# Performance work log

Hardware: AMD Instinct MI355X
Metric: run time of the kernel (lower is better)

## Reference

```python
import math
import jax, jax.numpy as jnp
import numpy as np

B, I, D, H, K, MAXI, FF = 2, 1024, 1024, 16, 64, 1024, 4096
DH = D // H
EPS = 1e-5

def _ln(x, g, b):
    m = x.mean(-1, keepdims=True)
    v = ((x - m) ** 2).mean(-1, keepdims=True)
    return (x - m) / jnp.sqrt(v + EPS) * g + b

def setup_inputs() -> dict:
    key = jax.random.key(0)
    ks = jax.random.split(key, 16)
    p = lambda i, sh: (0.02 * jax.random.normal(ks[i], sh)).astype(jnp.float32)
    # clamped relative-position indices: clamp(j - floor(1.0*i), -K, K) + K
    ar = np.arange(MAXI)
    idx = np.clip(ar[None, :] - ar[:, None], -K, K) + K  # [maxI, maxI]
    return {
        'x': jax.random.normal(ks[0], (B, I, D), dtype=jnp.float32),
        'j': jax.random.normal(ks[1], (B, I, D), dtype=jnp.float32),
        'ln1_g': jnp.ones((D,), jnp.float32), 'ln1_b': jnp.zeros((D,), jnp.float32),
        'Wv_w': p(2, (D, D)), 'Wv_b': jnp.zeros((D,), jnp.float32),
        'Wg_w': p(3, (D, D)), 'Wg_b': jnp.zeros((D,), jnp.float32),
        'lnv_g': jnp.ones((D,), jnp.float32), 'lnv_b': jnp.zeros((D,), jnp.float32),
        'Wq1_w': p(4, (D, D)), 'Wq1_b': jnp.zeros((D,), jnp.float32),
        'Wk_w': p(5, (D, D)), 'Wk_b': jnp.zeros((D,), jnp.float32),
        'Wq2_w': p(6, (D, D)), 'Wq2_b': jnp.zeros((D,), jnp.float32),
        'rel_emb': p(7, (2 * K + 1, D)),
        'Wo_w': p(8, (D, D)), 'Wo_b': jnp.zeros((D,), jnp.float32),
        'ln2_g': jnp.ones((D,), jnp.float32), 'ln2_b': jnp.zeros((D,), jnp.float32),
        'ff1_w': p(9, (D, FF)), 'ff1_b': jnp.zeros((FF,), jnp.float32),
        'ff2_w': p(10, (FF, D)), 'ff2_b': jnp.zeros((D,), jnp.float32),
        'indices': jnp.asarray(idx, jnp.int32),
    }

def reference(x, j, ln1_g, ln1_b, Wv_w, Wv_b, Wg_w, Wg_b, lnv_g, lnv_b,
              Wq1_w, Wq1_b, Wk_w, Wk_b, Wq2_w, Wq2_b, rel_emb,
              Wo_w, Wo_b, ln2_g, ln2_b, ff1_w, ff1_b, ff2_w, ff2_b, indices):
    Bv, Iq, _ = x.shape
    res = x
    xn = _ln(x, ln1_g, ln1_b)
    # value / gate streams with gelu activation, layernorm on v only
    v = _ln(jax.nn.gelu(xn @ Wv_w + Wv_b, approximate=False), lnv_g, lnv_b)
    g = jax.nn.gelu(xn @ Wg_w + Wg_b, approximate=False)
    vh = v.reshape(Bv, -1, H, DH)   # [B,J,H,Dh]
    gh = g.reshape(Bv, -1, H, DH)   # [B,I,H,Dh]
    # absolute-position scores: Q1(j) . K(j)^T
    q1 = (j @ Wq1_w + Wq1_b).reshape(Bv, -1, H, DH)
    kh = (j @ Wk_w + Wk_b).reshape(Bv, -1, H, DH)
    aa = jnp.einsum('bihd,bjhd->bhij', q1, kh)  # [B,H,I,J]
    # relative-position scores: Q2(j) . rel_embed^T, gathered by clamped indices
    q2 = (j @ Wq2_w + Wq2_b).reshape(Bv, -1, H, DH)
    rh = rel_emb.reshape(2 * K + 1, H, DH)
    arf = jnp.einsum('bihd,rhd->bhir', q2, rh)  # [B,H,I,2K+1]
    Jk = kh.shape[1]
    idx = jnp.broadcast_to(indices[None, None, :Iq, :Jk], (Bv, H, Iq, Jk))
    ar = jnp.take_along_axis(arf, idx, axis=-1)  # [B,H,I,J]
    a = jax.nn.softmax((aa + ar) / math.sqrt(DH), axis=-1)
    o = jnp.einsum('bhij,bjhd->bihd', a, vh) * gh  # gated attention output
    o = o.reshape(Bv, -1, D) @ Wo_w + Wo_b
    x1 = o + res
    # feed-forward sublayer
    h = jax.nn.relu(_ln(x1, ln2_g, ln2_b) @ ff1_w + ff1_b)
    out = h @ ff2_w + ff2_b + x1
    return (out, a)
```

## Files before the change

kernel.cpp:

```cpp
#include <hip/hip_runtime.h>
#include <hip/hip_bf16.h>
#include <math.h>

#define D_   1024
#define H_   16
#define DH_  64
#define FF_  4096
#define R_   129
#define I_   1024
#define B_   2
#define MROWS 2048
#define QKVLD 3072

typedef __bf16 v8bf16 __attribute__((ext_vector_type(8)));
typedef float f32x4 __attribute__((ext_vector_type(4)));

__device__ __forceinline__ float gelu_f(float x) {
    return 0.5f * x * (1.0f + erff(x * 0.7071067811865476f));
}

__device__ __forceinline__ void ldsld16(const void* g, void* l) {
    __builtin_amdgcn_global_load_lds(
        (const __attribute__((address_space(1))) void*)g,
        (__attribute__((address_space(3))) void*)l, 16, 0, 0);
}

__global__ __launch_bounds__(256) void cvt_bf16(const float* __restrict__ in,
        __hip_bfloat16* __restrict__ out, int n4) {
    int i = blockIdx.x * 256 + threadIdx.x;
    if (i >= n4) return;
    float4 v = reinterpret_cast<const float4*>(in)[i];
    union { __hip_bfloat16 h[4]; uint2 u; } pk;
    pk.h[0] = __float2bfloat16(v.x); pk.h[1] = __float2bfloat16(v.y);
    pk.h[2] = __float2bfloat16(v.z); pk.h[3] = __float2bfloat16(v.w);
    reinterpret_cast<uint2*>(out)[i] = pk.u;
}

__global__ __launch_bounds__(256) void cvt_rel_bias(const float* __restrict__ rel,
        __hip_bfloat16* __restrict__ relb,
        const float* __restrict__ q1b_, const float* __restrict__ kb_,
        const float* __restrict__ q2b_, const float* __restrict__ vb_,
        const float* __restrict__ gb_,
        float* __restrict__ bias3, float* __restrict__ bias2) {
    int bid = blockIdx.x, t = threadIdx.x;
    if (bid < 129) {
        int i = bid * 256 + t;
        float4 v = reinterpret_cast<const float4*>(rel)[i];
        union { __hip_bfloat16 h[4]; uint2 u; } pk;
        pk.h[0] = __float2bfloat16(v.x); pk.h[1] = __float2bfloat16(v.y);
        pk.h[2] = __float2bfloat16(v.z); pk.h[3] = __float2bfloat16(v.w);
        reinterpret_cast<uint2*>(relb)[i] = pk.u;
    } else {
        int k = bid - 129;
        const float* src = k == 0 ? q1b_ : k == 1 ? kb_ : k == 2 ? q2b_ : k == 3 ? vb_ : gb_;
        float* dst = (k < 3 ? bias3 + k * D_ : bias2 + (k - 3) * D_);
        reinterpret_cast<float4*>(dst)[t] = reinterpret_cast<const float4*>(src)[t];
    }
}

__global__ __launch_bounds__(256) void wtrans6(
        const float* __restrict__ s0, const float* __restrict__ s1,
        const float* __restrict__ s2, const float* __restrict__ s3,
        const float* __restrict__ s4, const float* __restrict__ s5,
        __hip_bfloat16* __restrict__ d0, __hip_bfloat16* __restrict__ d1,
        __hip_bfloat16* __restrict__ d2, __hip_bfloat16* __restrict__ d3,
        __hip_bfloat16* __restrict__ d4, __hip_bfloat16* __restrict__ d5) {
    __shared__ float T[64][65];
    int z = blockIdx.z;
    const float* W = z == 0 ? s0 : z == 1 ? s1 : z == 2 ? s2 : z == 3 ? s3 : z == 4 ? s4 : s5;
    __hip_bfloat16* WT = z == 0 ? d0 : z == 1 ? d1 : z == 2 ? d2 : z == 3 ? d3 : z == 4 ? d4 : d5;
    int k0 = blockIdx.y * 64, n0 = blockIdx.x * 64;
    int t = threadIdx.x;
#pragma unroll
    for (int i = 0; i < 16; i++) {
        int e = t + i * 256, r = e >> 6, c = e & 63;
        T[r][c] = W[(size_t)(k0 + r) * D_ + n0 + c];
    }
    __syncthreads();
#pragma unroll
    for (int i = 0; i < 16; i++) {
        int e = t + i * 256, r = e >> 6, c = e & 63;
        WT[(size_t)(n0 + r) * D_ + k0 + c] = __float2bfloat16(T[c][r]);
    }
}

__global__ __launch_bounds__(256) void wtrans_ff(
        const float* __restrict__ f1, const float* __restrict__ f2,
        __hip_bfloat16* __restrict__ d1, __hip_bfloat16* __restrict__ d2) {
    __shared__ float T[64][65];
    int z = blockIdx.z;
    const float* W = z == 0 ? f1 : f2;
    __hip_bfloat16* WT = z == 0 ? d1 : d2;
    int K = z == 0 ? D_ : FF_;
    int N = z == 0 ? FF_ : D_;
    int k0 = (z == 0 ? blockIdx.y : blockIdx.x) * 64;
    int n0 = (z == 0 ? blockIdx.x : blockIdx.y) * 64;
    int t = threadIdx.x;
#pragma unroll
    for (int i = 0; i < 16; i++) {
        int e = t + i * 256, r = e >> 6, c = e & 63;
        T[r][c] = W[(size_t)(k0 + r) * N + n0 + c];
    }
    __syncthreads();
#pragma unroll
    for (int i = 0; i < 16; i++) {
        int e = t + i * 256, r = e >> 6, c = e & 63;
        WT[(size_t)(n0 + r) * K + k0 + c] = __float2bfloat16(T[c][r]);
    }
}

__global__ __launch_bounds__(256) void vtrans(const float* __restrict__ v,
        __hip_bfloat16* __restrict__ vt) {
    __shared__ float T[64][65];
    int z = blockIdx.y, b = z >> 4, h = z & 15;
    int j0 = blockIdx.x * 64;
    int t = threadIdx.x;
#pragma unroll
    for (int i = 0; i < 16; i++) {
        int e = t + i * 256, r = e >> 6, c = e & 63;
        T[r][c] = v[(size_t)(b * I_ + j0 + r) * D_ + h * DH_ + c];
    }
    __syncthreads();
#pragma unroll
    for (int i = 0; i < 16; i++) {
        int e = t + i * 256, r = e >> 6, c = e & 63;
        vt[((size_t)z * DH_ + r) * I_ + j0 + c] = __float2bfloat16(T[c][r]);
    }
}

template<int MR, int NWC, int ACT, int RES, int OUTBF>
__global__ __launch_bounds__(256) void gemm_mfma(
        const __hip_bfloat16* __restrict__ A,
        const __hip_bfloat16* __restrict__ Bt,
        const float* __restrict__ bias,
        const float* __restrict__ res,
        void* __restrict__ Cout,
        int N, int Kd, int lda, int ldb, int ldc,
        size_t sAb, size_t sAh, size_t sBb, size_t sBh, size_t sCz) {
    constexpr int NWR = 4 / NWC;
    constexpr int BM = NWR * MR * 16;
    constexpr int BN = NWC * 64;
    __shared__ __align__(16) __hip_bfloat16 As[BM * 64];
    __shared__ __align__(16) __hip_bfloat16 Bs[BN * 64];
    const char* AsB = (const char*)As;
    const char* BsB = (const char*)Bs;
    int z = blockIdx.z;
    const __hip_bfloat16* Ab = A + (size_t)(z >> 4) * sAb + (size_t)(z & 15) * sAh;
    const __hip_bfloat16* Bb = Bt + (size_t)(z >> 4) * sBb + (size_t)(z & 15) * sBh;
    float* Cf = (float*)Cout + (size_t)z * sCz;
    __hip_bfloat16* Cb = (__hip_bfloat16*)Cout + (size_t)z * sCz;
    int m0 = blockIdx.y * BM, n0 = blockIdx.x * BN;
    int t = threadIdx.x;
    int l = t & 63, w = t >> 6;
    int wr = w / NWC, wc = w % NWC;
    int lr = l & 15, kq = l >> 4;
    int rx = lr & 7;

    f32x4 acc[MR][4] = {};

    for (int k0 = 0; k0 < Kd; k0 += 64) {
#pragma unroll
        for (int i = 0; i < BM / 32; i++) {
            int e = t + i * 256;
            int row = e >> 3, sl = e & 7;
            int kb = sl ^ (row & 7);
            ldsld16(Ab + (size_t)(m0 + row) * lda + (k0 + kb * 8), (void*)(AsB + e * 16));
        }
#pragma unroll
        for (int i = 0; i < BN / 32; i++) {
            int e = t + i * 256;
            int row = e >> 3, sl = e & 7;
            int kb = sl ^ (row & 7);
            int nr = n0 + row; if (nr > N - 1) nr = N - 1;
            ldsld16(Bb + (size_t)nr * ldb + (k0 + kb * 8), (void*)(BsB + e * 16));
        }
        __syncthreads();
#pragma unroll
        for (int kc = 0; kc < 2; kc++) {
            int sloff = (((kc << 2) + kq) ^ rx) << 4;
            v8bf16 af[MR], bfr[4];
#pragma unroll
            for (int mr = 0; mr < MR; mr++)
                af[mr] = *(const v8bf16*)(AsB + ((wr * (MR * 16) + mr * 16 + lr) << 7) + sloff);
#pragma unroll
            for (int nc = 0; nc < 4; nc++)
                bfr[nc] = *(const v8bf16*)(BsB + ((wc * 64 + nc * 16 + lr) << 7) + sloff);
#pragma unroll
            for (int mr = 0; mr < MR; mr++)
#pragma unroll
                for (int nc = 0; nc < 4; nc++)
                    acc[mr][nc] = __builtin_amdgcn_mfma_f32_16x16x32_bf16(
                        af[mr], bfr[nc], acc[mr][nc], 0, 0, 0);
        }
        __syncthreads();
    }

#pragma unroll
    for (int mr = 0; mr < MR; mr++) {
        int rbase = m0 + wr * (MR * 16) + mr * 16 + kq * 4;
#pragma unroll
        for (int nc = 0; nc < 4; nc++) {
            int col = n0 + wc * 64 + nc * 16 + lr;
            bool okc = col < N;
            float bv = (bias && okc) ? bias[col] : 0.f;
#pragma unroll
            for (int ri = 0; ri < 4; ri++) {
                int r = rbase + ri;
                float val = acc[mr][nc][ri] + bv;
                if (ACT == 1) val = gelu_f(val);
                if (ACT == 2) val = fmaxf(val, 0.f);
                if (RES) val += res[(size_t)r * ldc + col];
                if (okc) {
                    if (OUTBF == 2) {
                        if (col < D_) Cf[(size_t)r * ldc + col] = val;
                        else ((__hip_bfloat16*)res)[(size_t)r * ldc + (col - D_)] =
                                 __float2bfloat16(val);
                    } else if (OUTBF == 1) {
                        Cb[(size_t)r * ldc + col] = __float2bfloat16(val);
                    } else {
                        Cf[(size_t)r * ldc + col] = val;
                    }
                }
            }
        }
    }
}

#define F5_K  32512
#define F5_V  40704
#define F5_P  48896
#define SC2   0.1803368801111244f
__global__ __launch_bounds__(512) void flash_attn5(
        const __hip_bfloat16* __restrict__ qkv,
        const __hip_bfloat16* __restrict__ vt,
        const __hip_bfloat16* __restrict__ arfb,
        const __hip_bfloat16* __restrict__ gb,
        float* __restrict__ a_out,
        __hip_bfloat16* __restrict__ obuf) {
    __shared__ __align__(16) char lds[65280];
    __hip_bfloat16* arl = (__hip_bfloat16*)lds;
    char* kB = lds + F5_K;
    char* vB = lds + F5_V;
    char* pB = lds + F5_P;

    int z = blockIdx.y, b = z >> 4, h = z & 15;
    int i0 = blockIdx.x * 128;
    int t = threadIdx.x, l = t & 63, w = t >> 6;
    int lr = l & 15, kq = l >> 4;
    const __hip_bfloat16* Kg = qkv + (size_t)(b * I_) * QKVLD + D_ + h * DH_;
    const __hip_bfloat16* Vg = vt + (size_t)z * DH_ * I_;
    const __hip_bfloat16* arz = arfb + (size_t)z * I_ * R_;

#pragma unroll
    for (int i = 0; i < 2; i++) {
        int e = t + i * 512;
        int row = e >> 3, sl = e & 7;
        int kb = sl ^ (row & 7);
        ldsld16(qkv + (size_t)(b * I_ + i0 + row) * QKVLD + h * DH_ + kb * 8,
                (void*)(pB + e * 16));
    }
    for (int idx = t; idx < 128 * 127; idx += 512) {
        int row = idx / 127, rm = idx - row * 127;
        arl[idx] = arz[((size_t)(i0 + row)) * R_ + rm + 1];
    }
    __syncthreads();
    v8bf16 qf[2];
#pragma unroll
    for (int kc = 0; kc < 2; kc++)
        qf[kc] = *(const v8bf16*)(pB + ((w * 16 + lr) << 7) + ((((kc << 2) + kq) ^ (lr & 7)) << 4));

    int irow = w * 16 + kq * 4;
    int ig = i0 + irow;
    float loS[4], hiS[4];
#pragma unroll
    for (int ri = 0; ri < 4; ri++) {
        loS[ri] = __bfloat162float(arz[((size_t)(ig + ri)) * R_ + 0])   * SC2;
        hiS[ri] = __bfloat162float(arz[((size_t)(ig + ri)) * R_ + 128]) * SC2;
    }

    float l_ln[4] = {0.f, 0.f, 0.f, 0.f};
    for (int jt = 0; jt < 16; jt++) {
        int j0 = jt * 64;
        {
            int row = t >> 3, sl = t & 7;
            int kb = sl ^ (row & 7);
            ldsld16(Kg + (size_t)(j0 + row) * QKVLD + kb * 8, (void*)(kB + t * 16));
        }
        __syncthreads();
        f32x4 acc[4] = {};
        __builtin_amdgcn_s_setprio(1);
#pragma unroll
        for (int kc = 0; kc < 2; kc++) {
            int sloff = ((((kc << 2) + kq)) ^ (lr & 7)) << 4;
#pragma unroll
            for (int tt = 0; tt < 4; tt++) {
                v8bf16 kf = *(const v8bf16*)(kB + ((tt * 16 + lr) << 7) + sloff);
                acc[tt] = __builtin_amdgcn_mfma_f32_16x16x32_bf16(qf[kc], kf, acc[tt], 0, 0, 0);
            }
        }
        __builtin_amdgcn_s_setprio(0);
#pragma unroll
        for (int ri = 0; ri < 4; ri++) {
            int i_g = ig + ri;
            float sc[4];
            bool lo_all = (j0 + 63) <= (i_g - 64);
            bool hi_all = j0 >= (i_g + 64);
            if (lo_all || hi_all) {
                float c = lo_all ? loS[ri] : hiS[ri];
#pragma unroll
                for (int tt = 0; tt < 4; tt++) sc[tt] = fmaf(acc[tt][ri], SC2, c);
            } else {
#pragma unroll
                for (int tt = 0; tt < 4; tt++) {
                    int reln = j0 + tt * 16 + lr - i_g;
                    float arv = reln <= -64 ? loS[ri] : (reln >= 64 ? hiS[ri] :
                        __bfloat162float(arl[(irow + ri) * 127 + reln + 63]) * SC2);
                    sc[tt] = fmaf(acc[tt][ri], SC2, arv);
                }
            }
            l_ln[ri] += exp2f(sc[0]) + exp2f(sc[1]) + exp2f(sc[2]) + exp2f(sc[3]);
        }
        __syncthreads();
    }
    float offb[4];
#pragma unroll
    for (int ri = 0; ri < 4; ri++) {
        float s = l_ln[ri];
#pragma unroll
        for (int off = 1; off < 16; off <<= 1) s += __shfl_xor(s, off, 64);
        offb[ri] = __log2f(s);
    }

    f32x4 oacc[4] = {};
    for (int jt = 0; jt < 16; jt++) {
        int j0 = jt * 64;
        {
            int row = t >> 3, sl = t & 7;
            int kb = sl ^ (row & 7);
            ldsld16(Kg + (size_t)(j0 + row) * QKVLD + kb * 8, (void*)(kB + t * 16));
            ldsld16(Vg + (size_t)row * I_ + j0 + kb * 8, (void*)(vB + t * 16));
        }
        __syncthreads();
        f32x4 acc[4] = {};
        __builtin_amdgcn_s_setprio(1);
#pragma unroll
        for (int kc = 0; kc < 2; kc++) {
            int sloff = ((((kc << 2) + kq)) ^ (lr & 7)) << 4;
#pragma unroll
            for (int tt = 0; tt < 4; tt++) {
                v8bf16 kf = *(const v8bf16*)(kB + ((tt * 16 + lr) << 7) + sloff);
                acc[tt] = __builtin_amdgcn_mfma_f32_16x16x32_bf16(qf[kc], kf, acc[tt], 0, 0, 0);
            }
        }
        __builtin_amdgcn_s_setprio(0);
#pragma unroll
        for (int ri = 0; ri < 4; ri++) {
            int i_g = ig + ri;
            int rowl = irow + ri;
            float sc[4];
            bool lo_all = (j0 + 63) <= (i_g - 64);
            bool hi_all = j0 >= (i_g + 64);
            if (lo_all || hi_all) {
                float c = lo_all ? loS[ri] : hiS[ri];
#pragma unroll
                for (int tt = 0; tt < 4; tt++) sc[tt] = fmaf(acc[tt][ri], SC2, c);
            } else {
#pragma unroll
                for (int tt = 0; tt < 4; tt++) {
                    int reln = j0 + tt * 16 + lr - i_g;
                    float arv = reln <= -64 ? loS[ri] : (reln >= 64 ? hiS[ri] :
                        __bfloat162float(arl[rowl * 127 + reln + 63]) * SC2);
                    sc[tt] = fmaf(acc[tt][ri], SC2, arv);
                }
            }
            float* gout = a_out + ((size_t)z * I_ + i0 + rowl) * I_ + j0;
#pragma unroll
            for (int tt = 0; tt < 4; tt++) {
                float p = exp2f(sc[tt] - offb[ri]);
                __builtin_nontemporal_store(p, gout + tt * 16 + lr);
                *(__hip_bfloat16*)(pB + (rowl << 7) +
                        ((((tt * 2) + (lr >> 3)) ^ (rowl & 7)) << 4) + (lr & 7) * 2) =
                    __float2bfloat16(p);
            }
        }
        __syncthreads();
        __builtin_amdgcn_s_setprio(1);
#pragma unroll
        for (int kc = 0; kc < 2; kc++) {
            int sloff = ((((kc << 2) + kq)) ^ (lr & 7)) << 4;
            v8bf16 pf = *(const v8bf16*)(pB + ((w * 16 + lr) << 7) + sloff);
#pragma unroll
            for (int nc = 0; nc < 4; nc++) {
                v8bf16 vf = *(const v8bf16*)(vB + ((nc * 16 + lr) << 7) + sloff);
                oacc[nc] = __builtin_amdgcn_mfma_f32_16x16x32_bf16(pf, vf, oacc[nc], 0, 0, 0);
            }
        }
        __builtin_amdgcn_s_setprio(0);
        __syncthreads();
    }
#pragma unroll
    for (int nc = 0; nc < 4; nc++) {
#pragma unroll
        for (int ri = 0; ri < 4; ri++) {
            int r = i0 + irow + ri;
            size_t oi = ((size_t)(b * I_ + r)) * D_ + h * DH_ + nc * 16 + lr;
            obuf[oi] = __float2bfloat16(oacc[nc][ri] * __bfloat162float(gb[oi]));
        }
    }
}

template<int OUTBF>
__global__ __launch_bounds__(256) void ln_kernel(const float* __restrict__ in,
        void* __restrict__ out, const float* __restrict__ gw,
        const float* __restrict__ bw) {
    __shared__ float shs[4], shq[4];
    int row = blockIdx.x;
    int t = threadIdx.x;
    float4 v = reinterpret_cast<const float4*>(in + (size_t)row * D_)[t];
    float s = v.x + v.y + v.z + v.w;
#pragma unroll
    for (int off = 32; off > 0; off >>= 1) s += __shfl_down(s, off, 64);
    if ((t & 63) == 0) shs[t >> 6] = s;
    __syncthreads();
    float mean = (shs[0] + shs[1] + shs[2] + shs[3]) * (1.0f / D_);
    float d0 = v.x - mean, d1 = v.y - mean, d2 = v.z - mean, d3 = v.w - mean;
    float q = d0 * d0 + d1 * d1 + d2 * d2 + d3 * d3;
#pragma unroll
    for (int off = 32; off > 0; off >>= 1) q += __shfl_down(q, off, 64);
    if ((t & 63) == 0) shq[t >> 6] = q;
    __syncthreads();
    float var = (shq[0] + shq[1] + shq[2] + shq[3]) * (1.0f / D_);
    float rstd = rsqrtf(var + 1e-5f);
    float4 g4 = reinterpret_cast<const float4*>(gw)[t];
    float4 b4 = reinterpret_cast<const float4*>(bw)[t];
    float o0 = d0 * rstd * g4.x + b4.x;
    float o1 = d1 * rstd * g4.y + b4.y;
    float o2 = d2 * rstd * g4.z + b4.z;
    float o3 = d3 * rstd * g4.w + b4.w;
    if (OUTBF) {
        union { __hip_bfloat16 h[4]; uint2 u; } pk;
        pk.h[0] = __float2bfloat16(o0); pk.h[1] = __float2bfloat16(o1);
        pk.h[2] = __float2bfloat16(o2); pk.h[3] = __float2bfloat16(o3);
        reinterpret_cast<uint2*>((__hip_bfloat16*)out + (size_t)row * D_)[t] = pk.u;
    } else {
        float4 o; o.x = o0; o.y = o1; o.z = o2; o.w = o3;
        reinterpret_cast<float4*>((float*)out + (size_t)row * D_)[t] = o;
    }
}

extern "C" void kernel_launch(void* const* d_in, const int* in_sizes, int n_in,
                              void* d_out, int out_size, void* d_ws, size_t ws_size,
                              hipStream_t stream) {
    const float* x      = (const float*)d_in[0];
    const float* jin    = (const float*)d_in[1];
    const float* ln1_g  = (const float*)d_in[2];
    const float* ln1_b  = (const float*)d_in[3];
    const float* Wv_w   = (const float*)d_in[4];
    const float* Wv_b   = (const float*)d_in[5];
    const float* Wg_w   = (const float*)d_in[6];
    const float* Wg_b   = (const float*)d_in[7];
    const float* lnv_g  = (const float*)d_in[8];
    const float* lnv_b  = (const float*)d_in[9];
    const float* Wq1_w  = (const float*)d_in[10];
    const float* Wq1_b  = (const float*)d_in[11];
    const float* Wk_w   = (const float*)d_in[12];
    const float* Wk_b   = (const float*)d_in[13];
    const float* Wq2_w  = (const float*)d_in[14];
    const float* Wq2_b  = (const float*)d_in[15];
    const float* rel    = (const float*)d_in[16];
    const float* Wo_w   = (const float*)d_in[17];
    const float* Wo_b   = (const float*)d_in[18];
    const float* ln2_g  = (const float*)d_in[19];
    const float* ln2_b  = (const float*)d_in[20];
    const float* ff1_w  = (const float*)d_in[21];
    const float* ff1_b  = (const float*)d_in[22];
    const float* ff2_w  = (const float*)d_in[23];
    const float* ff2_b  = (const float*)d_in[24];

    float* out0  = (float*)d_out;
    float* a_out = out0 + (size_t)B_ * I_ * D_;

    char* wsb = (char*)d_ws;
    const size_t MB = 1u << 20;
    __hip_bfloat16* wvwgT= (__hip_bfloat16*)(wsb + 0 * MB);
    __hip_bfloat16* qkvT = (__hip_bfloat16*)(wsb + 4 * MB);
    __hip_bfloat16* WoT  = (__hip_bfloat16*)(wsb + 10 * MB);
    __hip_bfloat16* ff1T = (__hip_bfloat16*)(wsb + 12 * MB);
    __hip_bfloat16* ff2T = (__hip_bfloat16*)(wsb + 20 * MB);
    __hip_bfloat16* jbf  = (__hip_bfloat16*)(wsb + 28 * MB);
    __hip_bfloat16* qkv  = (__hip_bfloat16*)(wsb + 32 * MB);
    __hip_bfloat16* relb = (__hip_bfloat16*)(wsb + 44 * MB);
    __hip_bfloat16* arfb = (__hip_bfloat16*)(wsb + 45 * MB);
    __hip_bfloat16* gbuf = (__hip_bfloat16*)(wsb + 54 * MB);
    float*          vbuf = (float*)        (wsb + 58 * MB);
    __hip_bfloat16* xnb  = (__hip_bfloat16*)(wsb + 28 * MB);
    __hip_bfloat16* vt   = (__hip_bfloat16*)(wsb + 28 * MB);
    __hip_bfloat16* obuf = (__hip_bfloat16*)(wsb + 58 * MB);
    float*          x1   = (float*)        (wsb + 32 * MB);
    __hip_bfloat16* x1nb = (__hip_bfloat16*)(wsb + 40 * MB);
    __hip_bfloat16* hbuf = (__hip_bfloat16*)(wsb + 44 * MB);
    float*          bias3= (float*)        (wsb + 66 * MB);
    float*          bias2= (float*)        (wsb + 66 * MB + 16384);

    dim3 blk(256);

    cvt_bf16<<<2048, blk, 0, stream>>>(jin, jbf, (MROWS * D_) / 4);
    cvt_rel_bias<<<134, blk, 0, stream>>>(rel, relb,
        Wq1_b, Wk_b, Wq2_b, Wv_b, Wg_b, bias3, bias2);
    wtrans6<<<dim3(16, 16, 6), blk, 0, stream>>>(
        Wq1_w, Wk_w, Wq2_w, Wv_w, Wg_w, Wo_w,
        qkvT, qkvT + 1024*1024, qkvT + 2048*1024,
        wvwgT, wvwgT + 1024*1024, WoT);
    wtrans_ff<<<dim3(64, 16, 2), blk, 0, stream>>>(ff1_w, ff2_w, ff1T, ff2T);

    gemm_mfma<4, 2, 0, 0, 1><<<dim3(24, 16, 1), blk, 0, stream>>>(
        jbf, qkvT, bias3, nullptr, qkv, QKVLD, D_, D_, D_, QKVLD, 0, 0, 0, 0, 0);
    gemm_mfma<4, 2, 0, 0, 1><<<dim3(2, 8, 32), blk, 0, stream>>>(
        qkv + 2 * D_, relb, nullptr, nullptr, arfb,
        R_, DH_, QKVLD, D_, R_,
        (size_t)I_ * QKVLD, (size_t)DH_, 0, (size_t)DH_, (size_t)I_ * R_);

    ln_kernel<1><<<MROWS, blk, 0, stream>>>(x, xnb, ln1_g, ln1_b);
    gemm_mfma<4, 2, 1, 0, 2><<<dim3(16, 16, 1), blk, 0, stream>>>(
        xnb, wvwgT, bias2, (const float*)gbuf, vbuf, 2 * D_, D_, D_, D_, D_, 0, 0, 0, 0, 0);
    ln_kernel<0><<<MROWS, blk, 0, stream>>>(vbuf, vbuf, lnv_g, lnv_b);
    vtrans<<<dim3(16, 32), blk, 0, stream>>>(vbuf, vt);

    flash_attn5<<<dim3(8, 32), dim3(512), 0, stream>>>(qkv, vt, arfb, gbuf, a_out, obuf);

    gemm_mfma<2, 1, 0, 1, 0><<<dim3(16, 16, 1), blk, 0, stream>>>(
        obuf, WoT, Wo_b, x, x1, D_, D_, D_, D_, D_, 0, 0, 0, 0, 0);
    ln_kernel<1><<<MROWS, blk, 0, stream>>>(x1, x1nb, ln2_g, ln2_b);
    gemm_mfma<4, 2, 2, 0, 1><<<dim3(32, 16, 1), blk, 0, stream>>>(
        x1nb, ff1T, ff1_b, nullptr, hbuf, FF_, D_, D_, D_, FF_, 0, 0, 0, 0, 0);
    gemm_mfma<2, 1, 0, 1, 0><<<dim3(16, 16, 1), blk, 0, stream>>>(
        hbuf, ff2T, ff2_b, x1, out0, D_, FF_, FF_, FF_, D_, 0, 0, 0, 0, 0);
}
```

Baseline: 296.0 us.

## Shrink attention tiles to 64 query rows, double K/V chunk, retile QKV GEMMs

New measurement: 271.9 us. -8.1%, faster.

```diff
diff --git a/kernel.cpp b/kernel.cpp
--- a/kernel.cpp
+++ b/kernel.cpp
@@ -226,25 +226,24 @@
     }
 }
 
-#define F5_K  32512
-#define F5_V  40704
-#define F5_P  48896
+#define F6_K  0
+#define F6_V  16384
+#define F6_P  32768
 #define SC2   0.1803368801111244f
-__global__ __launch_bounds__(512) void flash_attn5(
+__global__ __launch_bounds__(256) void flash_attn6(
         const __hip_bfloat16* __restrict__ qkv,
         const __hip_bfloat16* __restrict__ vt,
         const __hip_bfloat16* __restrict__ arfb,
         const __hip_bfloat16* __restrict__ gb,
         float* __restrict__ a_out,
         __hip_bfloat16* __restrict__ obuf) {
-    __shared__ __align__(16) char lds[65280];
-    __hip_bfloat16* arl = (__hip_bfloat16*)lds;
-    char* kB = lds + F5_K;
-    char* vB = lds + F5_V;
-    char* pB = lds + F5_P;
+    __shared__ __align__(16) char lds[49152];
+    char* kB = lds + F6_K;
+    char* vB = lds + F6_V;
+    char* pB = lds + F6_P;
 
     int z = blockIdx.y, b = z >> 4, h = z & 15;
-    int i0 = blockIdx.x * 128;
+    int i0 = blockIdx.x * 64;
     int t = threadIdx.x, l = t & 63, w = t >> 6;
     int lr = l & 15, kq = l >> 4;
     const __hip_bfloat16* Kg = qkv + (size_t)(b * I_) * QKVLD + D_ + h * DH_;
@@ -253,16 +252,12 @@
 
 #pragma unroll
     for (int i = 0; i < 2; i++) {
-        int e = t + i * 512;
+        int e = t + i * 256;
         int row = e >> 3, sl = e & 7;
         int kb = sl ^ (row & 7);
         ldsld16(qkv + (size_t)(b * I_ + i0 + row) * QKVLD + h * DH_ + kb * 8,
                 (void*)(pB + e * 16));
     }
-    for (int idx = t; idx < 128 * 127; idx += 512) {
-        int row = idx / 127, rm = idx - row * 127;
-        arl[idx] = arz[((size_t)(i0 + row)) * R_ + rm + 1];
-    }
     __syncthreads();
     v8bf16 qf[2];
 #pragma unroll
@@ -279,46 +274,56 @@
     }
 
     float l_ln[4] = {0.f, 0.f, 0.f, 0.f};
-    for (int jt = 0; jt < 16; jt++) {
-        int j0 = jt * 64;
-        {
-            int row = t >> 3, sl = t & 7;
-            int kb = sl ^ (row & 7);
-            ldsld16(Kg + (size_t)(j0 + row) * QKVLD + kb * 8, (void*)(kB + t * 16));
-        }
-        __syncthreads();
-        f32x4 acc[4] = {};
-        __builtin_amdgcn_s_setprio(1);
-#pragma unroll
-        for (int kc = 0; kc < 2; kc++) {
-            int sloff = ((((kc << 2) + kq)) ^ (lr & 7)) << 4;
-#pragma unroll
-            for (int tt = 0; tt < 4; tt++) {
-                v8bf16 kf = *(const v8bf16*)(kB + ((tt * 16 + lr) << 7) + sloff);
-                acc[tt] = __builtin_amdgcn_mfma_f32_16x16x32_bf16(qf[kc], kf, acc[tt], 0, 0, 0);
-            }
-        }
-        __builtin_amdgcn_s_setprio(0);
-#pragma unroll
-        for (int ri = 0; ri < 4; ri++) {
-            int i_g = ig + ri;
-            float sc[4];
-            bool lo_all = (j0 + 63) <= (i_g - 64);
-            bool hi_all = j0 >= (i_g + 64);
-            if (lo_all || hi_all) {
-                float c = lo_all ? loS[ri] : hiS[ri];
-#pragma unroll
-                for (int tt = 0; tt < 4; tt++) sc[tt] = fmaf(acc[tt][ri], SC2, c);
-            } else {
+    for (int jp = 0; jp < 8; jp++) {
+#pragma unroll
+        for (int hf = 0; hf < 2; hf++) {
+#pragma unroll
+            for (int i = 0; i < 2; i++) {
+                int e = t + i * 256;
+                int row = e >> 3, sl = e & 7;
+                int kb = sl ^ (row & 7);
+                ldsld16(Kg + (size_t)((jp * 2 + hf) * 64 + row) * QKVLD + kb * 8,
+                        (void*)(kB + hf * 8192 + e * 16));
+            }
+        }
+        __syncthreads();
+#pragma unroll
+        for (int hf = 0; hf < 2; hf++) {
+            int j0 = (jp * 2 + hf) * 64;
+            const char* kBh = kB + hf * 8192;
+            f32x4 acc[4] = {};
+            __builtin_amdgcn_s_setprio(1);
+#pragma unroll
+            for (int kc = 0; kc < 2; kc++) {
+                int sloff = ((((kc << 2) + kq)) ^ (lr & 7)) << 4;
 #pragma unroll
                 for (int tt = 0; tt < 4; tt++) {
-                    int reln = j0 + tt * 16 + lr - i_g;
-                    float arv = reln <= -64 ? loS[ri] : (reln >= 64 ? hiS[ri] :
-                        __bfloat162float(arl[(irow + ri) * 127 + reln + 63]) * SC2);
-                    sc[tt] = fmaf(acc[tt][ri], SC2, arv);
-                }
-            }
-            l_ln[ri] += exp2f(sc[0]) + exp2f(sc[1]) + exp2f(sc[2]) + exp2f(sc[3]);
+                    v8bf16 kf = *(const v8bf16*)(kBh + ((tt * 16 + lr) << 7) + sloff);
+                    acc[tt] = __builtin_amdgcn_mfma_f32_16x16x32_bf16(qf[kc], kf, acc[tt], 0, 0, 0);
+                }
+            }
+            __builtin_amdgcn_s_setprio(0);
+#pragma unroll
+            for (int ri = 0; ri < 4; ri++) {
+                int i_g = ig + ri;
+                float sc[4];
+                bool lo_all = (j0 + 63) <= (i_g - 64);
+                bool hi_all = j0 >= (i_g + 64);
+                if (lo_all || hi_all) {
+                    float c = lo_all ? loS[ri] : hiS[ri];
+#pragma unroll
+                    for (int tt = 0; tt < 4; tt++) sc[tt] = fmaf(acc[tt][ri], SC2, c);
+                } else {
+#pragma unroll
+                    for (int tt = 0; tt < 4; tt++) {
+                        int reln = j0 + tt * 16 + lr - i_g;
+                        float arv = reln <= -64 ? loS[ri] : (reln >= 64 ? hiS[ri] :
+                            __bfloat162float(arz[(size_t)i_g * R_ + reln + 64]) * SC2);
+                        sc[tt] = fmaf(acc[tt][ri], SC2, arv);
+                    }
+                }
+                l_ln[ri] += exp2f(sc[0]) + exp2f(sc[1]) + exp2f(sc[2]) + exp2f(sc[3]);
+            }
         }
         __syncthreads();
     }
@@ -332,67 +337,82 @@
     }
 
     f32x4 oacc[4] = {};
-    for (int jt = 0; jt < 16; jt++) {
-        int j0 = jt * 64;
-        {
-            int row = t >> 3, sl = t & 7;
-            int kb = sl ^ (row & 7);
-            ldsld16(Kg + (size_t)(j0 + row) * QKVLD + kb * 8, (void*)(kB + t * 16));
-            ldsld16(Vg + (size_t)row * I_ + j0 + kb * 8, (void*)(vB + t * 16));
-        }
-        __syncthreads();
-        f32x4 acc[4] = {};
+    for (int jp = 0; jp < 8; jp++) {
+#pragma unroll
+        for (int hf = 0; hf < 2; hf++) {
+#pragma unroll
+            for (int i = 0; i < 2; i++) {
+                int e = t + i * 256;
+                int row = e >> 3, sl = e & 7;
+                int kb = sl ^ (row & 7);
+                ldsld16(Kg + (size_t)((jp * 2 + hf) * 64 + row) * QKVLD + kb * 8,
+                        (void*)(kB + hf * 8192 + e * 16));
+                ldsld16(Vg + (size_t)row * I_ + (jp * 2 + hf) * 64 + kb * 8,
+                        (void*)(vB + hf * 8192 + e * 16));
+            }
+        }
+        __syncthreads();
+#pragma unroll
+        for (int hf = 0; hf < 2; hf++) {
+            int j0 = (jp * 2 + hf) * 64;
+            const char* kBh = kB + hf * 8192;
+            char* pBh = pB + hf * 8192;
+            f32x4 acc[4] = {};
+            __builtin_amdgcn_s_setprio(1);
+#pragma unroll
+            for (int kc = 0; kc < 2; kc++) {
+                int sloff = ((((kc << 2) + kq)) ^ (lr & 7)) << 4;
+#pragma unroll
+                for (int tt = 0; tt < 4; tt++) {
+                    v8bf16 kf = *(const v8bf16*)(kBh + ((tt * 16 + lr) << 7) + sloff);
+                    acc[tt] = __builtin_amdgcn_mfma_f32_16x16x32_bf16(qf[kc], kf, acc[tt], 0, 0, 0);
+                }
+            }
+            __builtin_amdgcn_s_setprio(0);
+#pragma unroll
+            for (int ri = 0; ri < 4; ri++) {
+                int i_g = ig + ri;
+                int rowl = irow + ri;
+                float sc[4];
+                bool lo_all = (j0 + 63) <= (i_g - 64);
+                bool hi_all = j0 >= (i_g + 64);
+                if (lo_all || hi_all) {
+                    float c = lo_all ? loS[ri] : hiS[ri];
+#pragma unroll
+                    for (int tt = 0; tt < 4; tt++) sc[tt] = fmaf(acc[tt][ri], SC2, c);
+                } else {
+#pragma unroll
+                    for (int tt = 0; tt < 4; tt++) {
+                        int reln = j0 + tt * 16 + lr - i_g;
+                        float arv = reln <= -64 ? loS[ri] : (reln >= 64 ? hiS[ri] :
+                            __bfloat162float(arz[(size_t)i_g * R_ + reln + 64]) * SC2);
+                        sc[tt] = fmaf(acc[tt][ri], SC2, arv);
+                    }
+                }
+                float* gout = a_out + ((size_t)z * I_ + i0 + rowl) * I_ + j0;
+#pragma unroll
+                for (int tt = 0; tt < 4; tt++) {
+                    float p = exp2f(sc[tt] - offb[ri]);
+                    __builtin_nontemporal_store(p, gout + tt * 16 + lr);
+                    *(__hip_bfloat16*)(pBh + (rowl << 7) +
+                            ((((tt * 2) + (lr >> 3)) ^ (rowl & 7)) << 4) + (lr & 7) * 2) =
+                        __float2bfloat16(p);
+                }
+            }
+        }
+        __syncthreads();
         __builtin_amdgcn_s_setprio(1);
 #pragma unroll
-        for (int kc = 0; kc < 2; kc++) {
-            int sloff = ((((kc << 2) + kq)) ^ (lr & 7)) << 4;
-#pragma unroll
-            for (int tt = 0; tt < 4; tt++) {
-                v8bf16 kf = *(const v8bf16*)(kB + ((tt * 16 + lr) << 7) + sloff);
-                acc[tt] = __builtin_amdgcn_mfma_f32_16x16x32_bf16(qf[kc], kf, acc[tt], 0, 0, 0);
-            }
-        }
-        __builtin_amdgcn_s_setprio(0);
-#pragma unroll
-        for (int ri = 0; ri < 4; ri++) {
-            int i_g = ig + ri;
-            int rowl = irow + ri;
-            float sc[4];
-            bool lo_all = (j0 + 63) <= (i_g - 64);
-            bool hi_all = j0 >= (i_g + 64);
-            if (lo_all || hi_all) {
-                float c = lo_all ? loS[ri] : hiS[ri];
-#pragma unroll
-                for (int tt = 0; tt < 4; tt++) sc[tt] = fmaf(acc[tt][ri], SC2, c);
-            } else {
-#pragma unroll
-                for (int tt = 0; tt < 4; tt++) {
-                    int reln = j0 + tt * 16 + lr - i_g;
-                    float arv = reln <= -64 ? loS[ri] : (reln >= 64 ? hiS[ri] :
-                        __bfloat162float(arl[rowl * 127 + reln + 63]) * SC2);
-                    sc[tt] = fmaf(acc[tt][ri], SC2, arv);
-                }
-            }
-            float* gout = a_out + ((size_t)z * I_ + i0 + rowl) * I_ + j0;
-#pragma unroll
-            for (int tt = 0; tt < 4; tt++) {
-                float p = exp2f(sc[tt] - offb[ri]);
-                __builtin_nontemporal_store(p, gout + tt * 16 + lr);
-                *(__hip_bfloat16*)(pB + (rowl << 7) +
-                        ((((tt * 2) + (lr >> 3)) ^ (rowl & 7)) << 4) + (lr & 7) * 2) =
-                    __float2bfloat16(p);
-            }
-        }
-        __syncthreads();
-        __builtin_amdgcn_s_setprio(1);
-#pragma unroll
-        for (int kc = 0; kc < 2; kc++) {
-            int sloff = ((((kc << 2) + kq)) ^ (lr & 7)) << 4;
-            v8bf16 pf = *(const v8bf16*)(pB + ((w * 16 + lr) << 7) + sloff);
-#pragma unroll
-            for (int nc = 0; nc < 4; nc++) {
-                v8bf16 vf = *(const v8bf16*)(vB + ((nc * 16 + lr) << 7) + sloff);
-                oacc[nc] = __builtin_amdgcn_mfma_f32_16x16x32_bf16(pf, vf, oacc[nc], 0, 0, 0);
+        for (int hf = 0; hf < 2; hf++) {
+#pragma unroll
+            for (int kc = 0; kc < 2; kc++) {
+                int sloff = ((((kc << 2) + kq)) ^ (lr & 7)) << 4;
+                v8bf16 pf = *(const v8bf16*)(pB + hf * 8192 + ((w * 16 + lr) << 7) + sloff);
+#pragma unroll
+                for (int nc = 0; nc < 4; nc++) {
+                    v8bf16 vf = *(const v8bf16*)(vB + hf * 8192 + ((nc * 16 + lr) << 7) + sloff);
+                    oacc[nc] = __builtin_amdgcn_mfma_f32_16x16x32_bf16(pf, vf, oacc[nc], 0, 0, 0);
+                }
             }
         }
         __builtin_amdgcn_s_setprio(0);
@@ -513,7 +533,7 @@
         wvwgT, wvwgT + 1024*1024, WoT);
     wtrans_ff<<<dim3(64, 16, 2), blk, 0, stream>>>(ff1_w, ff2_w, ff1T, ff2T);
 
-    gemm_mfma<4, 2, 0, 0, 1><<<dim3(24, 16, 1), blk, 0, stream>>>(
+    gemm_mfma<2, 2, 0, 0, 1><<<dim3(24, 32, 1), blk, 0, stream>>>(
         jbf, qkvT, bias3, nullptr, qkv, QKVLD, D_, D_, D_, QKVLD, 0, 0, 0, 0, 0);
     gemm_mfma<4, 2, 0, 0, 1><<<dim3(2, 8, 32), blk, 0, stream>>>(
         qkv + 2 * D_, relb, nullptr, nullptr, arfb,
@@ -521,12 +541,12 @@
         (size_t)I_ * QKVLD, (size_t)DH_, 0, (size_t)DH_, (size_t)I_ * R_);
 
     ln_kernel<1><<<MROWS, blk, 0, stream>>>(x, xnb, ln1_g, ln1_b);
-    gemm_mfma<4, 2, 1, 0, 2><<<dim3(16, 16, 1), blk, 0, stream>>>(
+    gemm_mfma<2, 2, 1, 0, 2><<<dim3(16, 32, 1), blk, 0, stream>>>(
         xnb, wvwgT, bias2, (const float*)gbuf, vbuf, 2 * D_, D_, D_, D_, D_, 0, 0, 0, 0, 0);
     ln_kernel<0><<<MROWS, blk, 0, stream>>>(vbuf, vbuf, lnv_g, lnv_b);
     vtrans<<<dim3(16, 32), blk, 0, stream>>>(vbuf, vt);
 
-    flash_attn5<<<dim3(8, 32), dim3(512), 0, stream>>>(qkv, vt, arfb, gbuf, a_out, obuf);
+    flash_attn6<<<dim3(16, 32), blk, 0, stream>>>(qkv, vt, arfb, gbuf, a_out, obuf);
 
     gemm_mfma<2, 1, 0, 1, 0><<<dim3(16, 16, 1), blk, 0, stream>>>(
         obuf, WoT, Wo_b, x, x1, D_, D_, D_, D_, D_, 0, 0, 0, 0, 0);
```
